# Performance work log

Measured on AMD Instinct MI355X. Metric: run time of the kernel, lower is better.

Reference implementation:

```python
import jax, jax.numpy as jnp
import numpy as np

B, H, CO, NV, NQ = 16, 1024, 512, 2048, 2048

def setup_inputs() -> dict:
    key = jax.random.key(0)
    ks = jax.random.split(key, 7)
    return {
        "V": jax.random.normal(ks[0], (B, H, NV), dtype=jnp.float32),
        "Q": jax.random.normal(ks[1], (B, NQ, H), dtype=jnp.float32),
        "W_b": jax.random.normal(ks[2], (H, H), dtype=jnp.float32),
        "W_v": jax.random.normal(ks[3], (CO, H), dtype=jnp.float32),
        "W_q": jax.random.normal(ks[4], (CO, H), dtype=jnp.float32),
        "w_hv": jax.random.normal(ks[5], (CO, 1), dtype=jnp.float32),
        "w_hq": jax.random.normal(ks[6], (CO, 1), dtype=jnp.float32),
    }

def reference(V, Q, W_b, W_v, W_q, w_hv, w_hq):
    # C = Q @ (W_b @ V): [B, Nq, Nv]
    WbV = jnp.einsum('hk,bkv->bhv', W_b, V)
    C = jnp.einsum('bqh,bhv->bqv', Q, WbV)
    WvV = jnp.einsum('ch,bhv->bcv', W_v, V)          # [B, CO, Nv]
    WqQt = jnp.einsum('ch,bqh->bcq', W_q, Q)         # [B, CO, Nq]
    H_v = jnp.tanh(WvV + jnp.einsum('bcq,bqv->bcv', WqQt, C))   # [B, CO, Nv]
    H_q = jnp.tanh(WqQt + jnp.einsum('bcv,bqv->bcq', WvV, C))   # [B, CO, Nq]
    a_v = jax.nn.softmax(jnp.einsum('c,bcv->bv', w_hv[:, 0], H_v), axis=-1)[:, None, :]  # [B,1,Nv]
    a_q = jax.nn.softmax(jnp.einsum('c,bcq->bq', w_hq[:, 0], H_q), axis=-1)[:, None, :]  # [B,1,Nq]
    v = jnp.einsum('bv,bhv->bh', a_v[:, 0], V)   # [B, H]
    q = jnp.einsum('bq,bqh->bh', a_q[:, 0], Q)   # [B, H]
    return (a_v, a_q, v, q)
```

## Files before the change

kernel.cpp:

```cpp
#include <hip/hip_runtime.h>
#include <math.h>

#define Bn  16
#define Hd  1024
#define COn 512
#define NVn 2048
#define NQn 2048

#define BM 128
#define BN 128
#define BK 16
#define LDT 132

typedef unsigned short u16;
typedef __attribute__((ext_vector_type(8))) short short8;
typedef __attribute__((ext_vector_type(4))) float floatx4;

__device__ __forceinline__ float fast_tanh(float x) {
    float ax = fabsf(x);
    float e  = __expf(2.0f * ax);
    float t  = 1.0f - 2.0f / (e + 1.0f);
    return copysignf(t, x);
}

__device__ __forceinline__ u16 f32_to_bf16(float x) {
    unsigned u = __float_as_uint(x);
    unsigned r = (u + 0x7fffu + ((u >> 16) & 1u)) >> 16;
    return (u16)r;
}
__device__ __forceinline__ float bf16_to_f32(u16 h) {
    return __uint_as_float(((unsigned)h) << 16);
}

__device__ __forceinline__ void gload16(const u16* g, u16* l) {
    __builtin_amdgcn_global_load_lds(
        (__attribute__((address_space(1))) void*)(g),
        (__attribute__((address_space(3))) void*)(l), 16, 0, 0);
}

template <bool LOGITS>
__global__ __launch_bounds__(512, 2) void mm8p(
    const u16* __restrict__ Ahp, const u16* __restrict__ Alp, long batchA, int ldA,
    const u16* __restrict__ Bhp, const u16* __restrict__ Blp, long batchB, int ldB,
    int N, int K, int gx, int gy,
    const float* __restrict__ bias,
    u16* __restrict__ Ch, u16* __restrict__ Cl, long batchC,
    const float* __restrict__ w, float* __restrict__ logits)
{
    __shared__ u16 lds[2][4][256 * 32];

    const int tid = threadIdx.x;
    const int nwg = (int)gridDim.x;
    int bid = (int)blockIdx.x;
    {
        int q = nwg >> 3, r = nwg & 7, xcd = bid & 7, idx = bid >> 3;
        bid = (xcd < r ? xcd * (q + 1) : r * (q + 1) + (xcd - r) * q) + idx;
    }
    const int bpz = gx * gy;
    const int b    = bid / bpz;
    const int brem = bid - b * bpz;
    const int m0 = (brem / gx) * 256;
    const int n0 = (brem % gx) * 256;

    const u16* Ahb = Ahp + (long)b * batchA;
    const u16* Alb = Alp + (long)b * batchA;
    const u16* Bhb = Bhp + (long)b * batchB;
    const u16* Blb = Blp + (long)b * batchB;

    const int wave = tid >> 6, lane = tid & 63;
    const int quad = lane >> 4, l16 = lane & 15;
    const int xsl = (quad ^ ((l16 >> 1) & 3)) * 8;
    const int wm = (wave >> 2) * 128;
    const int wn = (wave & 3) * 64;

    const int smat  = wave >> 1;
    const int srow0 = (wave & 1) * 128;
    const int srl   = lane >> 2;
    const int kx    = ((lane & 3) ^ ((lane >> 3) & 3)) * 8;
    const u16* srcp = smat == 0 ? Ahb : smat == 1 ? Alb : smat == 2 ? Bhb : Blb;
    const long sld  = (smat < 2) ? ldA : ldB;
    const int rowbase = (smat < 2) ? m0 : n0;
    const u16* sp = srcp + (long)(rowbase + srow0 + srl) * sld + kx;

    floatx4 acc[8][4] = {};

#pragma unroll
    for (int j = 0; j < 8; ++j)
        gload16(sp + (long)j * 16 * sld, &lds[0][smat][(srow0 + j * 16) * 32]);
    asm volatile("s_waitcnt vmcnt(0)" ::: "memory");
    __builtin_amdgcn_s_barrier();

    const int NT = K >> 5;
    for (int t = 0; t < NT; ++t) {
        const int  cur = t & 1;
        const bool pf  = (t + 1 < NT);
        const long k0n = (long)(t + 1) * 32;
        const u16* Ah_ = &lds[cur][0][0];
        const u16* Al_ = &lds[cur][1][0];
        const u16* Bh_ = &lds[cur][2][0];
        const u16* Bl_ = &lds[cur][3][0];

        short8 bh[4], bl[4];
#pragma unroll
        for (int nt = 0; nt < 4; ++nt) {
            const int bs = (wn + nt * 16 + l16) * 32 + xsl;
            bh[nt] = *(const short8*)&Bh_[bs];
            bl[nt] = *(const short8*)&Bl_[bs];
        }
        if (pf) {
            u16* dst = &lds[cur ^ 1][smat][srow0 * 32];
#pragma unroll
            for (int j = 0; j < 8; ++j)
                gload16(sp + (long)j * 16 * sld + k0n, dst + j * 16 * 32);
        }
#pragma unroll
        for (int p = 0; p < 4; ++p) {
            const int as0 = (wm + p * 32 + l16) * 32 + xsl;
            const int as1 = as0 + 16 * 32;
            const short8 a0h = *(const short8*)&Ah_[as0];
            const short8 a0l = *(const short8*)&Al_[as0];
            const short8 a1h = *(const short8*)&Ah_[as1];
            const short8 a1l = *(const short8*)&Al_[as1];
            __builtin_amdgcn_s_setprio(1);
#pragma unroll
            for (int nt = 0; nt < 4; ++nt) {
                floatx4 c0 = acc[2 * p][nt];
                c0 = __builtin_amdgcn_mfma_f32_16x16x32_bf16(a0h, bh[nt], c0, 0, 0, 0);
                c0 = __builtin_amdgcn_mfma_f32_16x16x32_bf16(a0h, bl[nt], c0, 0, 0, 0);
                c0 = __builtin_amdgcn_mfma_f32_16x16x32_bf16(a0l, bh[nt], c0, 0, 0, 0);
                acc[2 * p][nt] = c0;
                floatx4 c1 = acc[2 * p + 1][nt];
                c1 = __builtin_amdgcn_mfma_f32_16x16x32_bf16(a1h, bh[nt], c1, 0, 0, 0);
                c1 = __builtin_amdgcn_mfma_f32_16x16x32_bf16(a1h, bl[nt], c1, 0, 0, 0);
                c1 = __builtin_amdgcn_mfma_f32_16x16x32_bf16(a1l, bh[nt], c1, 0, 0, 0);
                acc[2 * p + 1][nt] = c1;
            }
            __builtin_amdgcn_s_setprio(0);
        }
        if (pf) asm volatile("s_waitcnt vmcnt(0)" ::: "memory");
        __builtin_amdgcn_s_barrier();
    }

    if constexpr (!LOGITS) {
        u16* Chb = Ch + (long)b * batchC;
        u16* Clb = Cl + (long)b * batchC;
#pragma unroll
        for (int mt = 0; mt < 8; ++mt)
#pragma unroll
            for (int nt = 0; nt < 4; ++nt)
#pragma unroll
                for (int r = 0; r < 4; ++r) {
                    const int row = m0 + wm + mt * 16 + quad * 4 + r;
                    const int col = n0 + wn + nt * 16 + l16;
                    float x = acc[mt][nt][r];
                    if (bias) x += bias[(long)row * N + col];
                    const u16 h = f32_to_bf16(x);
                    Chb[(long)row * N + col] = h;
                    Clb[(long)row * N + col] = f32_to_bf16(x - bf16_to_f32(h));
                }
    } else {
        float cs[4] = {};
#pragma unroll
        for (int nt = 0; nt < 4; ++nt)
#pragma unroll
            for (int mt = 0; mt < 8; ++mt)
#pragma unroll
                for (int r = 0; r < 4; ++r) {
                    const int row = m0 + wm + mt * 16 + quad * 4 + r;
                    cs[nt] = fmaf(w[row], fast_tanh(acc[mt][nt][r]), cs[nt]);
                }
        float* red = (float*)&lds[0][0][0];
        const int r8 = (wave >> 2) * 4 + quad;
#pragma unroll
        for (int nt = 0; nt < 4; ++nt)
            red[r8 * 256 + wn + nt * 16 + l16] = cs[nt];
        __syncthreads();
        if (tid < 256) {
            float s = 0.f;
#pragma unroll
            for (int r = 0; r < 8; ++r) s += red[r * 256 + tid];
            atomicAdd(logits + (long)b * N + n0 + tid, s);
        }
    }
}

template <bool LOGITS>
__global__ __launch_bounds__(256) void mm3(
    const u16* __restrict__ Ahp, const u16* __restrict__ Alp, long batchA, int ldA,
    const u16* __restrict__ Bhp, const u16* __restrict__ Blp, long batchB, int ldB,
    int N, int K,
    const float* __restrict__ bias,
    u16* __restrict__ Ch, u16* __restrict__ Cl, long batchC,
    const float* __restrict__ w, float* __restrict__ logits)
{
    __shared__ u16 Ah[128 * 32], Al[128 * 32], Bh[128 * 32], Bl[128 * 32];
    const int tid = threadIdx.x;
    const int b   = blockIdx.z;
    const int m0  = blockIdx.y * 128;
    const int n0  = blockIdx.x * 128;
    const u16* Ahb = Ahp + (long)b * batchA;
    const u16* Alb = Alp + (long)b * batchA;
    const u16* Bhb = Bhp + (long)b * batchB;
    const u16* Blb = Blp + (long)b * batchB;
    const int wave = tid >> 6, lane = tid & 63, quad = lane >> 4, l16 = lane & 15;
    const int xsl = (quad ^ ((l16 >> 1) & 3)) * 8;
    const int wm = (wave >> 1) * 64, wn = (wave & 1) * 64;
    floatx4 acc[4][4] = {};

    for (int k0 = 0; k0 < K; k0 += 32) {
#pragma unroll
        for (int i = 0; i < 2; ++i) {
            int c = i * 256 + tid;
            int row = c >> 2, u = c & 3;
            int g = u ^ ((row >> 1) & 3);
            long ga = (long)(m0 + row) * ldA + k0 + g * 8;
            long gb = (long)(n0 + row) * ldB + k0 + g * 8;
            *(short8*)&Ah[row * 32 + u * 8] = *(const short8*)&Ahb[ga];
            *(short8*)&Al[row * 32 + u * 8] = *(const short8*)&Alb[ga];
            *(short8*)&Bh[row * 32 + u * 8] = *(const short8*)&Bhb[gb];
            *(short8*)&Bl[row * 32 + u * 8] = *(const short8*)&Blb[gb];
        }
        __syncthreads();
        short8 ah[4], al[4], bh[4], bl[4];
#pragma unroll
        for (int t4 = 0; t4 < 4; ++t4) {
            const int as = (wm + t4 * 16 + l16) * 32 + xsl;
            ah[t4] = *(const short8*)&Ah[as];
            al[t4] = *(const short8*)&Al[as];
            const int bs = (wn + t4 * 16 + l16) * 32 + xsl;
            bh[t4] = *(const short8*)&Bh[bs];
            bl[t4] = *(const short8*)&Bl[bs];
        }
#pragma unroll
        for (int mt = 0; mt < 4; ++mt)
#pragma unroll
            for (int nt = 0; nt < 4; ++nt) {
                floatx4 a0 = acc[mt][nt];
                a0 = __builtin_amdgcn_mfma_f32_16x16x32_bf16(ah[mt], bh[nt], a0, 0, 0, 0);
                a0 = __builtin_amdgcn_mfma_f32_16x16x32_bf16(ah[mt], bl[nt], a0, 0, 0, 0);
                a0 = __builtin_amdgcn_mfma_f32_16x16x32_bf16(al[mt], bh[nt], a0, 0, 0, 0);
                acc[mt][nt] = a0;
            }
        __syncthreads();
    }

    if constexpr (!LOGITS) {
        u16* Chb = Ch + (long)b * batchC;
        u16* Clb = Cl + (long)b * batchC;
#pragma unroll
        for (int mt = 0; mt < 4; ++mt)
#pragma unroll
            for (int nt = 0; nt < 4; ++nt)
#pragma unroll
                for (int r = 0; r < 4; ++r) {
                    int row = m0 + wm + mt * 16 + quad * 4 + r;
                    int col = n0 + wn + nt * 16 + l16;
                    float x = acc[mt][nt][r];
                    if (bias) x += bias[(long)row * N + col];
                    u16 h = f32_to_bf16(x);
                    u16 l = f32_to_bf16(x - bf16_to_f32(h));
                    Chb[(long)row * N + col] = h;
                    Clb[(long)row * N + col] = l;
                }
    } else {
        float cs[4] = {};
#pragma unroll
        for (int nt = 0; nt < 4; ++nt)
#pragma unroll
            for (int mt = 0; mt < 4; ++mt)
#pragma unroll
                for (int r = 0; r < 4; ++r) {
                    int row = m0 + wm + mt * 16 + quad * 4 + r;
                    cs[nt] = fmaf(w[row], fast_tanh(acc[mt][nt][r]), cs[nt]);
                }
        float* red = (float*)Ah;
        const int r8 = (wave >> 1) * 4 + quad;
#pragma unroll
        for (int nt = 0; nt < 4; ++nt)
            red[r8 * 128 + wn + nt * 16 + l16] = cs[nt];
        __syncthreads();
        if (tid < 128) {
            float s = 0.f;
#pragma unroll
            for (int r = 0; r < 8; ++r) s += red[r * 128 + tid];
            atomicAdd(logits + (long)b * N + n0 + tid, s);
        }
    }
}

__global__ __launch_bounds__(256) void split_kernel(
    const float* __restrict__ X, u16* __restrict__ Xh, u16* __restrict__ Xl)
{
    long i0 = ((long)blockIdx.x * 256 + threadIdx.x) * 4;
    float4 v = *(const float4*)(X + i0);
    float xs[4] = {v.x, v.y, v.z, v.w};
    u16 h[4], l[4];
#pragma unroll
    for (int i = 0; i < 4; ++i) {
        h[i] = f32_to_bf16(xs[i]);
        l[i] = f32_to_bf16(xs[i] - bf16_to_f32(h[i]));
    }
    *(ushort4*)(Xh + i0) = *(ushort4*)h;
    *(ushort4*)(Xl + i0) = *(ushort4*)l;
}

__global__ __launch_bounds__(256) void tsplit_kernel(
    const float* __restrict__ src, u16* __restrict__ dh, u16* __restrict__ dl,
    int R, int C)
{
    __shared__ float tile[64][65];
    const int b = blockIdx.z;
    const int r0 = blockIdx.x * 64, c0 = blockIdx.y * 64;
    const float* S = src + (long)b * R * C;
    const int t = threadIdx.x;
    const int lr = t >> 2, lc0 = (t & 3) * 16;
#pragma unroll
    for (int i = 0; i < 4; ++i)
        *(float4*)&tile[lr][lc0 + i * 4] =
            *(const float4*)(S + (long)(r0 + lr) * C + c0 + lc0 + i * 4);
    __syncthreads();
    u16 hbuf[16], lbuf[16];
#pragma unroll
    for (int i = 0; i < 16; ++i) {
        float x = tile[lc0 + i][lr];
        u16 hi = f32_to_bf16(x);
        hbuf[i] = hi;
        lbuf[i] = f32_to_bf16(x - bf16_to_f32(hi));
    }
    long o = (long)b * R * C + (long)(c0 + lr) * R + r0 + lc0;
    *(short8*)(dh + o)     = *(short8*)&hbuf[0];
    *(short8*)(dh + o + 8) = *(short8*)&hbuf[8];
    *(short8*)(dl + o)     = *(short8*)&lbuf[0];
    *(short8*)(dl + o + 8) = *(short8*)&lbuf[8];
}

template <bool LOGITS>
__global__ __launch_bounds__(256) void gemm_core(
    const float* __restrict__ A, const float* __restrict__ Bm, float* __restrict__ C,
    const float* __restrict__ bias,
    int M, int N, int K,
    int sAm, int sAk, long batchA,
    int sBk, int sBn, long batchB,
    long batchC,
    const float* __restrict__ w, float* __restrict__ logits)
{
    __shared__ float As[BK][LDT];
    __shared__ float Bs[BK][LDT];
    const int tid = threadIdx.x;
    const int b   = blockIdx.z;
    const int m0  = blockIdx.y * BM;
    const int n0  = blockIdx.x * BN;
    const float* Ab = A  + (long)b * batchA;
    const float* Bb = Bm + (long)b * batchB;
    const int tm = tid >> 4, tn = tid & 15;
    float acc[8][8] = {};

    for (int k0 = 0; k0 < K; k0 += BK) {
        if (sAk == 1) {
#pragma unroll
            for (int i = 0; i < 2; ++i) {
                int idx = tid + i * 256;
                int m = idx >> 2, kg = (idx & 3) * 4;
                float4 v = *(const float4*)(Ab + (long)(m0 + m) * sAm + k0 + kg);
                As[kg+0][m] = v.x; As[kg+1][m] = v.y; As[kg+2][m] = v.z; As[kg+3][m] = v.w;
            }
        } else {
#pragma unroll
            for (int i = 0; i < 2; ++i) {
                int idx = tid + i * 256;
                int k = idx >> 5, mg = (idx & 31) * 4;
                float4 v = *(const float4*)(Ab + (long)(k0 + k) * sAk + m0 + mg);
                *(float4*)&As[k][mg] = v;
            }
        }
        if (sBn == 1) {
#pragma unroll
            for (int i = 0; i < 2; ++i) {
                int idx = tid + i * 256;
                int k = idx >> 5, ng = (idx & 31) * 4;
                float4 v = *(const float4*)(Bb + (long)(k0 + k) * sBk + n0 + ng);
                *(float4*)&Bs[k][ng] = v;
            }
        } else {
#pragma unroll
            for (int i = 0; i < 2; ++i) {
                int idx = tid + i * 256;
                int n = idx >> 2, kg = (idx & 3) * 4;
                float4 v = *(const float4*)(Bb + (long)(n0 + n) * sBn + k0 + kg);
                Bs[kg+0][n] = v.x; Bs[kg+1][n] = v.y; Bs[kg+2][n] = v.z; Bs[kg+3][n] = v.w;
            }
        }
        __syncthreads();
#pragma unroll
        for (int kk = 0; kk < BK; ++kk) {
            float a[8], bv[8];
            *(float4*)&a[0]  = *(const float4*)&As[kk][tm * 4];
            *(float4*)&a[4]  = *(const float4*)&As[kk][64 + tm * 4];
            *(float4*)&bv[0] = *(const float4*)&Bs[kk][tn * 4];
            *(float4*)&bv[4] = *(const float4*)&Bs[kk][64 + tn * 4];
#pragma unroll
            for (int i = 0; i < 8; ++i)
#pragma unroll
                for (int j = 0; j < 8; ++j)
                    acc[i][j] = fmaf(a[i], bv[j], acc[i][j]);
        }
        __syncthreads();
    }

    if constexpr (!LOGITS) {
        float* Cb = C + (long)b * batchC;
#pragma unroll
        for (int i = 0; i < 8; ++i) {
            int row = m0 + (i >> 2) * 64 + tm * 4 + (i & 3);
            float* crow = Cb + (long)row * N + n0;
            float4 o0 = {acc[i][0], acc[i][1], acc[i][2], acc[i][3]};
            float4 o1 = {acc[i][4], acc[i][5], acc[i][6], acc[i][7]};
            if (bias) {
                const float* brow = bias + (long)row * N + n0;
                float4 b0 = *(const float4*)(brow + tn * 4);
                float4 b1 = *(const float4*)(brow + 64 + tn * 4);
                o0.x += b0.x; o0.y += b0.y; o0.z += b0.z; o0.w += b0.w;
                o1.x += b1.x; o1.y += b1.y; o1.z += b1.z; o1.w += b1.w;
            }
            *(float4*)(crow + tn * 4) = o0;
            *(float4*)(crow + 64 + tn * 4) = o1;
        }
    } else {
        float wv[8];
#pragma unroll
        for (int i = 0; i < 8; ++i) wv[i] = w[m0 + (i >> 2) * 64 + tm * 4 + (i & 3)];
        float cs[8];
#pragma unroll
        for (int j = 0; j < 8; ++j) {
            float s = 0.f;
#pragma unroll
            for (int i = 0; i < 8; ++i) s = fmaf(wv[i], fast_tanh(acc[i][j]), s);
            cs[j] = s;
        }
        __syncthreads();
        *(float4*)&As[tm][tn * 4]      = *(float4*)&cs[0];
        *(float4*)&As[tm][64 + tn * 4] = *(float4*)&cs[4];
        __syncthreads();
        if (tid < 128) {
            float s = 0.f;
#pragma unroll
            for (int r = 0; r < 16; ++r) s += As[r][tid];
            atomicAdd(logits + (long)b * N + n0 + tid, s);
        }
    }
}

__global__ __launch_bounds__(256) void softmax_kernel(
    const float* __restrict__ lv, const float* __restrict__ lq, float* __restrict__ out)
{
    const int b = blockIdx.x;
    const int which = blockIdx.y;
    const float* x = (which == 0 ? lv : lq) + (long)b * 2048;
    float* o = out + (long)which * (Bn * 2048) + (long)b * 2048;
    const int tid = threadIdx.x;
    __shared__ float sm[4], ss[4];

    float m = -3.4e38f;
    for (int i = tid; i < 2048; i += 256) m = fmaxf(m, x[i]);
    for (int off = 32; off > 0; off >>= 1) m = fmaxf(m, __shfl_down(m, off));
    if ((tid & 63) == 0) sm[tid >> 6] = m;
    __syncthreads();
    m = fmaxf(fmaxf(sm[0], sm[1]), fmaxf(sm[2], sm[3]));

    float s = 0.f;
    for (int i = tid; i < 2048; i += 256) s += expf(x[i] - m);
    for (int off = 32; off > 0; off >>= 1) s += __shfl_down(s, off);
    if ((tid & 63) == 0) ss[tid >> 6] = s;
    __syncthreads();
    s = ss[0] + ss[1] + ss[2] + ss[3];
    float inv = 1.0f / s;
    for (int i = tid; i < 2048; i += 256) o[i] = expf(x[i] - m) * inv;
}

__global__ __launch_bounds__(256) void vout_kernel(
    const float* __restrict__ V, const float* __restrict__ av, float* __restrict__ vout)
{
    const int wave = threadIdx.x >> 6, lane = threadIdx.x & 63;
    const long idx = (long)blockIdx.x * 4 + wave;
    const int b = (int)(idx >> 10);
    const int h = (int)(idx & 1023);
    const float* vp = V + ((long)b * Hd + h) * NVn;
    const float* ap = av + (long)b * NVn;
    float s = 0.f;
    for (int i = lane; i < NVn; i += 64) s = fmaf(ap[i], vp[i], s);
    for (int off = 32; off > 0; off >>= 1) s += __shfl_down(s, off);
    if (lane == 0) vout[idx] = s;
}

__global__ __launch_bounds__(256) void qout_kernel(
    const float* __restrict__ Q, const float* __restrict__ aq, float* __restrict__ qout)
{
    const int h  = blockIdx.x * 256 + threadIdx.x;
    const int b  = blockIdx.z;
    const int q0 = blockIdx.y * 256;
    const float* qp = Q + (long)b * NQn * Hd;
    const float* ap = aq + (long)b * NQn + q0;
    float s = 0.f;
    for (int q = 0; q < 256; ++q) s = fmaf(ap[q], qp[(long)(q0 + q) * Hd + h], s);
    atomicAdd(qout + (long)b * Hd + h, s);
}

extern "C" void kernel_launch(void* const* d_in, const int* in_sizes, int n_in,
                              void* d_out, int out_size, void* d_ws, size_t ws_size,
                              hipStream_t stream) {
    const float* V    = (const float*)d_in[0];
    const float* Q    = (const float*)d_in[1];
    const float* W_b  = (const float*)d_in[2];
    const float* W_v  = (const float*)d_in[3];
    const float* W_q  = (const float*)d_in[4];
    const float* w_hv = (const float*)d_in[5];
    const float* w_hq = (const float*)d_in[6];
    float* out = (float*)d_out;
    dim3 blk(256);

    const long BIG  = (long)Bn * Hd * NVn;
    const long GEL  = (long)Bn * Hd * Hd;
    const long TEL  = (long)Bn * COn * Hd;
    const long WQE  = (long)COn * Hd;
    const long WBE  = (long)Hd * Hd;

    u16* ws16 = (u16*)d_ws;
    u16* R1h  = ws16;            u16* R1l  = R1h + BIG;
    u16* Gh   = R1l + BIG;       u16* Gl   = Gh + GEL;
    u16* Th   = Gl + GEL;        u16* Tl   = Th + TEL;
    u16* Uh   = Gh;              u16* Ul   = Gh + TEL;
    u16* Wqh  = Tl + TEL;        u16* Wql  = Wqh + WQE;
    u16* Wvh  = Wql + WQE;       u16* Wvl  = Wvh + WQE;
    u16* Wbh  = Wvl + WQE;       u16* Wbl  = Wbh + WBE;
    u16* WbTh = Wbl + WBE;       u16* WbTl = WbTh + WBE;
    float* lv = (float*)(WbTl + WBE);
    float* lq = lv + Bn * NVn;
    const size_t need = (size_t)((u16*)(lq + Bn * NQn) - ws16) * 2;

    float* vout_p = out + 2 * Bn * NVn;
    float* qout_p = vout_p + Bn * Hd;

    if (ws_size >= need) {
        hipMemsetAsync(lv, 0, (size_t)(Bn * NVn + Bn * NQn) * sizeof(float), stream);
        hipMemsetAsync(qout_p, 0, (size_t)Bn * Hd * sizeof(float), stream);

        split_kernel<<<dim3((unsigned)(WQE / 1024)), blk, 0, stream>>>(W_q, Wqh, Wql);
        split_kernel<<<dim3((unsigned)(WQE / 1024)), blk, 0, stream>>>(W_v, Wvh, Wvl);
        split_kernel<<<dim3((unsigned)(WBE / 1024)), blk, 0, stream>>>(W_b, Wbh, Wbl);
        tsplit_kernel<<<dim3(Hd / 64, Hd / 64, 1), blk, 0, stream>>>(W_b, WbTh, WbTl, Hd, Hd);

        tsplit_kernel<<<dim3(NQn / 64, Hd / 64, Bn), blk, 0, stream>>>(Q, R1h, R1l, NQn, Hd);
        mm8p<false><<<dim3((Hd / 256) * (Hd / 256) * Bn), dim3(512), 0, stream>>>(
            R1h, R1l, (long)Hd * NQn, NQn,  R1h, R1l, (long)Hd * NQn, NQn,
            Hd, NQn, Hd / 256, Hd / 256,
            nullptr, Gh, Gl, (long)Hd * Hd, nullptr, nullptr);
        mm3<false><<<dim3(Hd / 128, COn / 128, Bn), blk, 0, stream>>>(
            Wqh, Wql, 0L, Hd,  Gh, Gl, (long)Hd * Hd, Hd,
            Hd, Hd, nullptr, Th, Tl, (long)COn * Hd, nullptr, nullptr);
        mm3<false><<<dim3(Hd / 128, COn / 128, Bn), blk, 0, stream>>>(
            Th, Tl, (long)COn * Hd, Hd,  WbTh, WbTl, 0L, Hd,
            Hd, Hd, W_v, Uh, Ul, (long)COn * Hd, nullptr, nullptr);
        tsplit_kernel<<<dim3(Hd / 64, NVn / 64, Bn), blk, 0, stream>>>(V, R1h, R1l, Hd, NVn);
        mm8p<true><<<dim3((NVn / 256) * (COn / 256) * Bn), dim3(512), 0, stream>>>(
            Uh, Ul, (long)COn * Hd, Hd,  R1h, R1l, (long)NVn * Hd, Hd,
            NVn, Hd, NVn / 256, COn / 256,
            nullptr, nullptr, nullptr, 0L, w_hv, lv);

        split_kernel<<<dim3((unsigned)(BIG / 1024)), blk, 0, stream>>>(V, R1h, R1l);
        mm8p<false><<<dim3((Hd / 256) * (Hd / 256) * Bn), dim3(512), 0, stream>>>(
            R1h, R1l, (long)Hd * NVn, NVn,  R1h, R1l, (long)Hd * NVn, NVn,
            Hd, NVn, Hd / 256, Hd / 256,
            nullptr, Gh, Gl, (long)Hd * Hd, nullptr, nullptr);
        mm3<false><<<dim3(Hd / 128, COn / 128, Bn), blk, 0, stream>>>(
            Wvh, Wvl, 0L, Hd,  Gh, Gl, (long)Hd * Hd, Hd,
            Hd, Hd, nullptr, Th, Tl, (long)COn * Hd, nullptr, nullptr);
        mm3<false><<<dim3(Hd / 128, COn / 128, Bn), blk, 0, stream>>>(
            Th, Tl, (long)COn * Hd, Hd,  Wbh, Wbl, 0L, Hd,
            Hd, Hd, W_q, Uh, Ul, (long)COn * Hd, nullptr, nullptr);
        split_kernel<<<dim3((unsigned)(BIG / 1024)), blk, 0, stream>>>(Q, R1h, R1l);
        mm8p<true><<<dim3((NQn / 256) * (COn / 256) * Bn), dim3(512), 0, stream>>>(
            Uh, Ul, (long)COn * Hd, Hd,  R1h, R1l, (long)NQn * Hd, Hd,
            NQn, Hd, NQn / 256, COn / 256,
            nullptr, nullptr, nullptr, 0L, w_hq, lq);

        softmax_kernel<<<dim3(Bn, 2), blk, 0, stream>>>(lv, lq, out);
        vout_kernel<<<dim3(Bn * Hd / 4), blk, 0, stream>>>(V, out, vout_p);
        qout_kernel<<<dim3(Hd / 256, NQn / 256, Bn), blk, 0, stream>>>(Q, out + Bn * NVn, qout_p);
        return;
    }

    float* ws = (float*)d_ws;
    float* g  = ws;
    float* t  = g + GEL;
    float* u  = t + TEL;
    float* flv = u + TEL;
    float* flq = flv + Bn * NVn;

    hipMemsetAsync(flv, 0, (size_t)(Bn * NVn + Bn * NQn) * sizeof(float), stream);
    hipMemsetAsync(qout_p, 0, (size_t)Bn * Hd * sizeof(float), stream);

    gemm_core<false><<<dim3(Hd/BN, Hd/BM, Bn), blk, 0, stream>>>(Q, Q, g, nullptr,
        Hd, Hd, NQn, 1, Hd, (long)NQn*Hd, Hd, 1, (long)NQn*Hd, (long)Hd*Hd, nullptr, nullptr);
    gemm_core<false><<<dim3(Hd/BN, COn/BM, Bn), blk, 0, stream>>>(W_q, g, t, nullptr,
        COn, Hd, Hd, Hd, 1, 0L, Hd, 1, (long)Hd*Hd, (long)COn*Hd, nullptr, nullptr);
    gemm_core<false><<<dim3(Hd/BN, COn/BM, Bn), blk, 0, stream>>>(t, W_b, u, W_v,
        COn, Hd, Hd, Hd, 1, (long)COn*Hd, Hd, 1, 0L, (long)COn*Hd, nullptr, nullptr);
    gemm_core<true><<<dim3(NVn/BN, COn/BM, Bn), blk, 0, stream>>>(
        u, V, nullptr, nullptr, COn, NVn, Hd,
        Hd, 1, (long)COn*Hd, NVn, 1, (long)Hd*NVn, 0L, w_hv, flv);
    gemm_core<false><<<dim3(Hd/BN, Hd/BM, Bn), blk, 0, stream>>>(V, V, g, nullptr,
        Hd, Hd, NVn, NVn, 1, (long)Hd*NVn, 1, NVn, (long)Hd*NVn, (long)Hd*Hd, nullptr, nullptr);
    gemm_core<false><<<dim3(Hd/BN, COn/BM, Bn), blk, 0, stream>>>(W_v, g, t, nullptr,
        COn, Hd, Hd, Hd, 1, 0L, Hd, 1, (long)Hd*Hd, (long)COn*Hd, nullptr, nullptr);
    gemm_core<false><<<dim3(Hd/BN, COn/BM, Bn), blk, 0, stream>>>(t, W_b, u, W_q,
        COn, Hd, Hd, Hd, 1, (long)COn*Hd, 1, Hd, 0L, (long)COn*Hd, nullptr, nullptr);
    gemm_core<true><<<dim3(NQn/BN, COn/BM, Bn), blk, 0, stream>>>(
        u, Q, nullptr, nullptr, COn, NQn, Hd,
        Hd, 1, (long)COn*Hd, 1, Hd, (long)NQn*Hd, 0L, w_hq, flq);

    softmax_kernel<<<dim3(Bn, 2), blk, 0, stream>>>(flv, flq, out);
    vout_kernel<<<dim3(Bn * Hd / 4), blk, 0, stream>>>(V, out, vout_p);
    qout_kernel<<<dim3(Hd / 256, NQn / 256, Bn), blk, 0, stream>>>(Q, out + Bn * NVn, qout_p);
}
```

Measured before the change: 1.257 ms.

## Double-buffer mm3 GEMM with direct global-to-LDS loads; fuse Q transpose and split

Replaces the mm3 GEMM with mm4. mm4 double-buffers LDS and prefetches the next K-tile with gload16 (direct global-to-LDS), one wave per operand matrix, while MFMAs run on the current tile under raised wave priority. It also adds tsplit2_kernel, which reads Q once and writes both the transposed and untransposed bf16 hi/lo splits, removing a later split_kernel pass over Q. The cost is an extra workspace buffer (R2h/R2l) and a larger workspace requirement, which could push execution onto the fallback path if ws_size is too small.

```diff
diff --git a/kernel.cpp b/kernel.cpp
--- a/kernel.cpp
+++ b/kernel.cpp
@@ -184,16 +184,15 @@
     }
 }
 
-template <bool LOGITS>
-__global__ __launch_bounds__(256) void mm3(
+__global__ __launch_bounds__(256, 2) void mm4(
     const u16* __restrict__ Ahp, const u16* __restrict__ Alp, long batchA, int ldA,
     const u16* __restrict__ Bhp, const u16* __restrict__ Blp, long batchB, int ldB,
     int N, int K,
     const float* __restrict__ bias,
-    u16* __restrict__ Ch, u16* __restrict__ Cl, long batchC,
-    const float* __restrict__ w, float* __restrict__ logits)
-{
-    __shared__ u16 Ah[128 * 32], Al[128 * 32], Bh[128 * 32], Bl[128 * 32];
+    u16* __restrict__ Ch, u16* __restrict__ Cl, long batchC)
+{
+    __shared__ u16 lds[2][4][128 * 32];
+
     const int tid = threadIdx.x;
     const int b   = blockIdx.z;
     const int m0  = blockIdx.y * 128;
@@ -202,35 +201,50 @@
     const u16* Alb = Alp + (long)b * batchA;
     const u16* Bhb = Bhp + (long)b * batchB;
     const u16* Blb = Blp + (long)b * batchB;
-    const int wave = tid >> 6, lane = tid & 63, quad = lane >> 4, l16 = lane & 15;
+
+    const int wave = tid >> 6, lane = tid & 63;
+    const int quad = lane >> 4, l16 = lane & 15;
     const int xsl = (quad ^ ((l16 >> 1) & 3)) * 8;
     const int wm = (wave >> 1) * 64, wn = (wave & 1) * 64;
+
+    const int smat = wave;
+    const int kx   = ((lane & 3) ^ ((lane >> 3) & 3)) * 8;
+    const u16* srcp = smat == 0 ? Ahb : smat == 1 ? Alb : smat == 2 ? Bhb : Blb;
+    const long sld  = (smat < 2) ? ldA : ldB;
+    const int rowbase = (smat < 2) ? m0 : n0;
+    const u16* sp = srcp + (long)(rowbase + (lane >> 2)) * sld + kx;
+
     floatx4 acc[4][4] = {};
 
-    for (int k0 = 0; k0 < K; k0 += 32) {
-#pragma unroll
-        for (int i = 0; i < 2; ++i) {
-            int c = i * 256 + tid;
-            int row = c >> 2, u = c & 3;
-            int g = u ^ ((row >> 1) & 3);
-            long ga = (long)(m0 + row) * ldA + k0 + g * 8;
-            long gb = (long)(n0 + row) * ldB + k0 + g * 8;
-            *(short8*)&Ah[row * 32 + u * 8] = *(const short8*)&Ahb[ga];
-            *(short8*)&Al[row * 32 + u * 8] = *(const short8*)&Alb[ga];
-            *(short8*)&Bh[row * 32 + u * 8] = *(const short8*)&Bhb[gb];
-            *(short8*)&Bl[row * 32 + u * 8] = *(const short8*)&Blb[gb];
-        }
-        __syncthreads();
+#pragma unroll
+    for (int j = 0; j < 8; ++j)
+        gload16(sp + (long)j * 16 * sld, &lds[0][smat][j * 16 * 32]);
+    asm volatile("s_waitcnt vmcnt(0)" ::: "memory");
+    __builtin_amdgcn_s_barrier();
+
+    const int NT = K >> 5;
+    for (int t = 0; t < NT; ++t) {
+        const int  cur = t & 1;
+        const bool pf  = (t + 1 < NT);
+        const long k0n = (long)(t + 1) * 32;
+
         short8 ah[4], al[4], bh[4], bl[4];
 #pragma unroll
         for (int t4 = 0; t4 < 4; ++t4) {
             const int as = (wm + t4 * 16 + l16) * 32 + xsl;
-            ah[t4] = *(const short8*)&Ah[as];
-            al[t4] = *(const short8*)&Al[as];
+            ah[t4] = *(const short8*)&lds[cur][0][as];
+            al[t4] = *(const short8*)&lds[cur][1][as];
             const int bs = (wn + t4 * 16 + l16) * 32 + xsl;
-            bh[t4] = *(const short8*)&Bh[bs];
-            bl[t4] = *(const short8*)&Bl[bs];
-        }
+            bh[t4] = *(const short8*)&lds[cur][2][bs];
+            bl[t4] = *(const short8*)&lds[cur][3][bs];
+        }
+        if (pf) {
+            u16* dst = &lds[cur ^ 1][smat][0];
+#pragma unroll
+            for (int j = 0; j < 8; ++j)
+                gload16(sp + (long)j * 16 * sld + k0n, dst + j * 16 * 32);
+        }
+        __builtin_amdgcn_s_setprio(1);
 #pragma unroll
         for (int mt = 0; mt < 4; ++mt)
 #pragma unroll
@@ -241,51 +255,28 @@
                 a0 = __builtin_amdgcn_mfma_f32_16x16x32_bf16(al[mt], bh[nt], a0, 0, 0, 0);
                 acc[mt][nt] = a0;
             }
-        __syncthreads();
-    }
-
-    if constexpr (!LOGITS) {
-        u16* Chb = Ch + (long)b * batchC;
-        u16* Clb = Cl + (long)b * batchC;
-#pragma unroll
-        for (int mt = 0; mt < 4; ++mt)
-#pragma unroll
-            for (int nt = 0; nt < 4; ++nt)
-#pragma unroll
-                for (int r = 0; r < 4; ++r) {
-                    int row = m0 + wm + mt * 16 + quad * 4 + r;
-                    int col = n0 + wn + nt * 16 + l16;
-                    float x = acc[mt][nt][r];
-                    if (bias) x += bias[(long)row * N + col];
-                    u16 h = f32_to_bf16(x);
-                    u16 l = f32_to_bf16(x - bf16_to_f32(h));
-                    Chb[(long)row * N + col] = h;
-                    Clb[(long)row * N + col] = l;
-                }
-    } else {
-        float cs[4] = {};
+        __builtin_amdgcn_s_setprio(0);
+        if (pf) asm volatile("s_waitcnt vmcnt(0)" ::: "memory");
+        __builtin_amdgcn_s_barrier();
+    }
+
+    u16* Chb = Ch + (long)b * batchC;
+    u16* Clb = Cl + (long)b * batchC;
+#pragma unroll
+    for (int mt = 0; mt < 4; ++mt)
 #pragma unroll
         for (int nt = 0; nt < 4; ++nt)
 #pragma unroll
-            for (int mt = 0; mt < 4; ++mt)
-#pragma unroll
-                for (int r = 0; r < 4; ++r) {
-                    int row = m0 + wm + mt * 16 + quad * 4 + r;
-                    cs[nt] = fmaf(w[row], fast_tanh(acc[mt][nt][r]), cs[nt]);
-                }
-        float* red = (float*)Ah;
-        const int r8 = (wave >> 1) * 4 + quad;
-#pragma unroll
-        for (int nt = 0; nt < 4; ++nt)
-            red[r8 * 128 + wn + nt * 16 + l16] = cs[nt];
-        __syncthreads();
-        if (tid < 128) {
-            float s = 0.f;
-#pragma unroll
-            for (int r = 0; r < 8; ++r) s += red[r * 128 + tid];
-            atomicAdd(logits + (long)b * N + n0 + tid, s);
-        }
-    }
+            for (int r = 0; r < 4; ++r) {
+                int row = m0 + wm + mt * 16 + quad * 4 + r;
+                int col = n0 + wn + nt * 16 + l16;
+                float x = acc[mt][nt][r];
+                if (bias) x += bias[(long)row * N + col];
+                u16 h = f32_to_bf16(x);
+                u16 l = f32_to_bf16(x - bf16_to_f32(h));
+                Chb[(long)row * N + col] = h;
+                Clb[(long)row * N + col] = l;
+            }
 }
 
 __global__ __launch_bounds__(256) void split_kernel(
@@ -332,6 +323,58 @@
     *(short8*)(dh + o + 8) = *(short8*)&hbuf[8];
     *(short8*)(dl + o)     = *(short8*)&lbuf[0];
     *(short8*)(dl + o + 8) = *(short8*)&lbuf[8];
+}
+
+__global__ __launch_bounds__(256) void tsplit2_kernel(
+    const float* __restrict__ src,
+    u16* __restrict__ dTh, u16* __restrict__ dTl,
+    u16* __restrict__ dh,  u16* __restrict__ dl,
+    int R, int C)
+{
+    __shared__ float tile[64][65];
+    const int b = blockIdx.z;
+    const int r0 = blockIdx.x * 64, c0 = blockIdx.y * 64;
+    const float* S = src + (long)b * R * C;
+    const int t = threadIdx.x;
+    const int lr = t >> 2, lc0 = (t & 3) * 16;
+    float4 v[4];
+#pragma unroll
+    for (int i = 0; i < 4; ++i) {
+        v[i] = *(const float4*)(S + (long)(r0 + lr) * C + c0 + lc0 + i * 4);
+        *(float4*)&tile[lr][lc0 + i * 4] = v[i];
+    }
+    {
+        u16 sh[16], sl[16];
+#pragma unroll
+        for (int i = 0; i < 4; ++i) {
+            float xs[4] = {v[i].x, v[i].y, v[i].z, v[i].w};
+#pragma unroll
+            for (int j = 0; j < 4; ++j) {
+                u16 hi = f32_to_bf16(xs[j]);
+                sh[i * 4 + j] = hi;
+                sl[i * 4 + j] = f32_to_bf16(xs[j] - bf16_to_f32(hi));
+            }
+        }
+        long os = (long)b * R * C + (long)(r0 + lr) * C + c0 + lc0;
+        *(short8*)(dh + os)     = *(short8*)&sh[0];
+        *(short8*)(dh + os + 8) = *(short8*)&sh[8];
+        *(short8*)(dl + os)     = *(short8*)&sl[0];
+        *(short8*)(dl + os + 8) = *(short8*)&sl[8];
+    }
+    __syncthreads();
+    u16 hbuf[16], lbuf[16];
+#pragma unroll
+    for (int i = 0; i < 16; ++i) {
+        float x = tile[lc0 + i][lr];
+        u16 hi = f32_to_bf16(x);
+        hbuf[i] = hi;
+        lbuf[i] = f32_to_bf16(x - bf16_to_f32(hi));
+    }
+    long o = (long)b * R * C + (long)(c0 + lr) * R + r0 + lc0;
+    *(short8*)(dTh + o)     = *(short8*)&hbuf[0];
+    *(short8*)(dTh + o + 8) = *(short8*)&hbuf[8];
+    *(short8*)(dTl + o)     = *(short8*)&lbuf[0];
+    *(short8*)(dTl + o + 8) = *(short8*)&lbuf[8];
 }
 
 template <bool LOGITS>
@@ -526,7 +569,8 @@
 
     u16* ws16 = (u16*)d_ws;
     u16* R1h  = ws16;            u16* R1l  = R1h + BIG;
-    u16* Gh   = R1l + BIG;       u16* Gl   = Gh + GEL;
+    u16* R2h  = R1l + BIG;       u16* R2l  = R2h + BIG;
+    u16* Gh   = R2l + BIG;       u16* Gl   = Gh + GEL;
     u16* Th   = Gl + GEL;        u16* Tl   = Th + TEL;
     u16* Uh   = Gh;              u16* Ul   = Gh + TEL;
     u16* Wqh  = Tl + TEL;        u16* Wql  = Wqh + WQE;
@@ -549,17 +593,18 @@
         split_kernel<<<dim3((unsigned)(WBE / 1024)), blk, 0, stream>>>(W_b, Wbh, Wbl);
         tsplit_kernel<<<dim3(Hd / 64, Hd / 64, 1), blk, 0, stream>>>(W_b, WbTh, WbTl, Hd, Hd);
 
-        tsplit_kernel<<<dim3(NQn / 64, Hd / 64, Bn), blk, 0, stream>>>(Q, R1h, R1l, NQn, Hd);
+        tsplit2_kernel<<<dim3(NQn / 64, Hd / 64, Bn), blk, 0, stream>>>(
+            Q, R1h, R1l, R2h, R2l, NQn, Hd);
         mm8p<false><<<dim3((Hd / 256) * (Hd / 256) * Bn), dim3(512), 0, stream>>>(
             R1h, R1l, (long)Hd * NQn, NQn,  R1h, R1l, (long)Hd * NQn, NQn,
             Hd, NQn, Hd / 256, Hd / 256,
             nullptr, Gh, Gl, (long)Hd * Hd, nullptr, nullptr);
-        mm3<false><<<dim3(Hd / 128, COn / 128, Bn), blk, 0, stream>>>(
+        mm4<<<dim3(Hd / 128, COn / 128, Bn), blk, 0, stream>>>(
             Wqh, Wql, 0L, Hd,  Gh, Gl, (long)Hd * Hd, Hd,
-            Hd, Hd, nullptr, Th, Tl, (long)COn * Hd, nullptr, nullptr);
-        mm3<false><<<dim3(Hd / 128, COn / 128, Bn), blk, 0, stream>>>(
+            Hd, Hd, nullptr, Th, Tl, (long)COn * Hd);
+        mm4<<<dim3(Hd / 128, COn / 128, Bn), blk, 0, stream>>>(
             Th, Tl, (long)COn * Hd, Hd,  WbTh, WbTl, 0L, Hd,
-            Hd, Hd, W_v, Uh, Ul, (long)COn * Hd, nullptr, nullptr);
+            Hd, Hd, W_v, Uh, Ul, (long)COn * Hd);
         tsplit_kernel<<<dim3(Hd / 64, NVn / 64, Bn), blk, 0, stream>>>(V, R1h, R1l, Hd, NVn);
         mm8p<true><<<dim3((NVn / 256) * (COn / 256) * Bn), dim3(512), 0, stream>>>(
             Uh, Ul, (long)COn * Hd, Hd,  R1h, R1l, (long)NVn * Hd, Hd,
@@ -571,15 +616,14 @@
             R1h, R1l, (long)Hd * NVn, NVn,  R1h, R1l, (long)Hd * NVn, NVn,
             Hd, NVn, Hd / 256, Hd / 256,
             nullptr, Gh, Gl, (long)Hd * Hd, nullptr, nullptr);
-        mm3<false><<<dim3(Hd / 128, COn / 128, Bn), blk, 0, stream>>>(
+        mm4<<<dim3(Hd / 128, COn / 128, Bn), blk, 0, stream>>>(
             Wvh, Wvl, 0L, Hd,  Gh, Gl, (long)Hd * Hd, Hd,
-            Hd, Hd, nullptr, Th, Tl, (long)COn * Hd, nullptr, nullptr);
-        mm3<false><<<dim3(Hd / 128, COn / 128, Bn), blk, 0, stream>>>(
+            Hd, Hd, nullptr, Th, Tl, (long)COn * Hd);
+        mm4<<<dim3(Hd / 128, COn / 128, Bn), blk, 0, stream>>>(
             Th, Tl, (long)COn * Hd, Hd,  Wbh, Wbl, 0L, Hd,
-            Hd, Hd, W_q, Uh, Ul, (long)COn * Hd, nullptr, nullptr);
-        split_kernel<<<dim3((unsigned)(BIG / 1024)), blk, 0, stream>>>(Q, R1h, R1l);
+            Hd, Hd, W_q, Uh, Ul, (long)COn * Hd);
         mm8p<true><<<dim3((NQn / 256) * (COn / 256) * Bn), dim3(512), 0, stream>>>(
-            Uh, Ul, (long)COn * Hd, Hd,  R1h, R1l, (long)NQn * Hd, Hd,
+            Uh, Ul, (long)COn * Hd, Hd,  R2h, R2l, (long)NQn * Hd, Hd,
             NQn, Hd, NQn / 256, COn / 256,
             nullptr, nullptr, nullptr, 0L, w_hq, lq);
 
```

Measured after the change: 1.204 ms. 1.04x faster.
